# Kernel optimization log

Hardware: AMD Instinct MI355X
Metric: run time of the kernel (lower is better)

## Reference

```python
import jax, jax.numpy as jnp
import numpy as np

NUM_ITEMS = 1_000_000
DIM = 64
NUM_HEADS = 2
TEMPERATURE = 0.1
BATCH = 4096
MAX_LEN = 200
PAD_FRAC = 0.3  # fraction of positions set to padding (-1)


def setup_inputs() -> dict:
    key = jax.random.key(0)
    k_tab, k_q, k_hist, k_pad = jax.random.split(key, 4)
    item_table = jax.random.normal(k_tab, (NUM_ITEMS, DIM), dtype=jnp.float32)
    queries = 0.1 * jax.random.normal(k_q, (NUM_HEADS, DIM), dtype=jnp.float32)
    hist = jax.random.randint(k_hist, (BATCH, MAX_LEN), 0, NUM_ITEMS, dtype=jnp.int32)
    pad = jax.random.uniform(k_pad, (BATCH, MAX_LEN)) < PAD_FRAC
    history_indices = jnp.where(pad, jnp.int32(-1), hist)
    return {"history_indices": history_indices, "item_table": item_table, "queries": queries}


def reference(history_indices, item_table, queries) -> jnp.ndarray:
    num_items = item_table.shape[0]
    num_heads = queries.shape[0]
    hi = jnp.clip(history_indices, -1, num_items - 1)
    lookup = jnp.where(hi == -1, 0, hi)
    hist_embs = item_table[lookup]                              # [B, L, D] gather
    scores = jnp.einsum('bld,kd->bkl', hist_embs, queries)      # [B, K, L]
    valid = (hi != -1)[:, None, :]                              # [B, 1, L]
    scores = jnp.where(valid, scores, jnp.float32(-1e9))
    attn = jax.nn.softmax(scores / TEMPERATURE, axis=-1)        # [B, K, L]
    head_vecs = jnp.einsum('bkl,bld->bkd', attn, hist_embs)     # [B, K, D]
    user_vec = head_vecs.mean(axis=1) * num_heads               # == sum over heads
    return user_vec
```

## Files before the change

kernel.cpp:

```cpp
#include <hip/hip_runtime.h>

#define NUM_ITEMS   1000000
#define DIM         64
#define BATCH       4096
#define MAX_LEN     200
#define INV_TEMP    10.0f
#define NEG_BIG     -1e9f

__global__ __launch_bounds__(512, 8)
void attn_pool_kernel(const int* __restrict__ hist,
                      const float* __restrict__ table,
                      const float* __restrict__ queries,
                      float* __restrict__ out)
{
    __shared__ int   hidx[MAX_LEN];
    __shared__ float mrg[8][16][11];

    const int b    = blockIdx.x;
    const int t    = threadIdx.x;
    const int lane = t & 63;
    const int wave = t >> 6;
    const int g    = t >> 4;
    const int c4   = t & 15;

    if (t < MAX_LEN) {
        int idx = hist[b * MAX_LEN + t];
        if (idx >= NUM_ITEMS) idx = NUM_ITEMS - 1;
        hidx[t] = idx;
    }
    __syncthreads();

    const float4 q0 = *reinterpret_cast<const float4*>(&queries[c4 * 4]);
    const float4 q1 = *reinterpret_cast<const float4*>(&queries[DIM + c4 * 4]);

    float  n0 = 0.f, n1 = 0.f;
    float4 a0 = {0.f, 0.f, 0.f, 0.f}, a1 = {0.f, 0.f, 0.f, 0.f};

    #pragma unroll
    for (int it = 0; it < (MAX_LEN + 31) / 32; ++it) {
        const int l = it * 32 + g;
        if (l < MAX_LEN) {
            const int idx = hidx[l];
            const int row = idx < 0 ? 0 : idx;
            const float4 v = *reinterpret_cast<const float4*>(
                &table[(size_t)row * DIM + c4 * 4]);
            float s0 = v.x * q0.x + v.y * q0.y + v.z * q0.z + v.w * q0.w;
            float s1 = v.x * q1.x + v.y * q1.y + v.z * q1.z + v.w * q1.w;
            #pragma unroll
            for (int off = 1; off < 16; off <<= 1) {
                s0 += __shfl_xor(s0, off);
                s1 += __shfl_xor(s1, off);
            }
            if (idx < 0) { s0 = NEG_BIG; s1 = NEG_BIG; }
            const float p0 = __expf(s0 * INV_TEMP);
            const float p1 = __expf(s1 * INV_TEMP);
            n0 += p0;
            a0.x += p0 * v.x;  a0.y += p0 * v.y;
            a0.z += p0 * v.z;  a0.w += p0 * v.w;
            n1 += p1;
            a1.x += p1 * v.x;  a1.y += p1 * v.y;
            a1.z += p1 * v.z;  a1.w += p1 * v.w;
        }
    }

    #pragma unroll
    for (int off = 16; off <= 32; off <<= 1) {
        n0   += __shfl_xor(n0,   off);
        a0.x += __shfl_xor(a0.x, off);  a0.y += __shfl_xor(a0.y, off);
        a0.z += __shfl_xor(a0.z, off);  a0.w += __shfl_xor(a0.w, off);
        n1   += __shfl_xor(n1,   off);
        a1.x += __shfl_xor(a1.x, off);  a1.y += __shfl_xor(a1.y, off);
        a1.z += __shfl_xor(a1.z, off);  a1.w += __shfl_xor(a1.w, off);
    }

    if (lane < 16) {
        float* s = mrg[wave][c4];
        s[0] = n0;
        s[1] = a0.x; s[2] = a0.y; s[3] = a0.z; s[4] = a0.w;
        s[5] = n1;
        s[6] = a1.x; s[7] = a1.y; s[8] = a1.z; s[9] = a1.w;
    }
    __syncthreads();

    if (t < 16) {
        float  N0 = 0.f, N1 = 0.f;
        float4 A0 = {0.f, 0.f, 0.f, 0.f}, A1 = {0.f, 0.f, 0.f, 0.f};
        #pragma unroll
        for (int w = 0; w < 8; ++w) {
            const float* s = mrg[w][t];
            N0   += s[0];
            A0.x += s[1];  A0.y += s[2];  A0.z += s[3];  A0.w += s[4];
            N1   += s[5];
            A1.x += s[6];  A1.y += s[7];  A1.z += s[8];  A1.w += s[9];
        }
        const float i0 = 1.f / N0, i1 = 1.f / N1;
        float4 o;
        o.x = A0.x * i0 + A1.x * i1;
        o.y = A0.y * i0 + A1.y * i1;
        o.z = A0.z * i0 + A1.z * i1;
        o.w = A0.w * i0 + A1.w * i1;
        *reinterpret_cast<float4*>(&out[b * DIM + t * 4]) = o;
    }
}

extern "C" void kernel_launch(void* const* d_in, const int* in_sizes, int n_in,
                              void* d_out, int out_size, void* d_ws, size_t ws_size,
                              hipStream_t stream) {
    const int*   hist    = (const int*)d_in[0];
    const float* table   = (const float*)d_in[1];
    const float* queries = (const float*)d_in[2];
    float*       out     = (float*)d_out;

    attn_pool_kernel<<<BATCH, 512, 0, stream>>>(hist, table, queries, out);
}
```

Baseline: 38.41 us.

## Map one wavefront per batch row and drop cross-wave shared-memory reduction

Each 64-lane wave now processes a whole batch row (4 rows per 256-thread block), iterating over all 200 history positions four at a time. This removes the cross-wave shared-memory merge and its second barrier. Padded positions now get a zero weight directly instead of exp(-1e9). The cost is less parallelism per row: each wave runs a 50-iteration serial loop, so the kernel relies on occupancy and unrolling to keep enough gathers in flight.

```diff
diff --git a/kernel.cpp b/kernel.cpp
--- a/kernel.cpp
+++ b/kernel.cpp
@@ -5,28 +5,33 @@
 #define BATCH       4096
 #define MAX_LEN     200
 #define INV_TEMP    10.0f
-#define NEG_BIG     -1e9f
 
-__global__ __launch_bounds__(512, 8)
+__global__ __launch_bounds__(256, 4)
 void attn_pool_kernel(const int* __restrict__ hist,
                       const float* __restrict__ table,
                       const float* __restrict__ queries,
                       float* __restrict__ out)
 {
-    __shared__ int   hidx[MAX_LEN];
-    __shared__ float mrg[8][16][11];
+    __shared__ int sidx[4][MAX_LEN];
 
-    const int b    = blockIdx.x;
     const int t    = threadIdx.x;
     const int lane = t & 63;
     const int wave = t >> 6;
-    const int g    = t >> 4;
-    const int c4   = t & 15;
+    const int b    = blockIdx.x * 4 + wave;
+    const int g    = lane >> 4;
+    const int c4   = lane & 15;
 
-    if (t < MAX_LEN) {
-        int idx = hist[b * MAX_LEN + t];
+    const int* hb = hist + (size_t)b * MAX_LEN;
+    #pragma unroll
+    for (int k = 0; k < 3; ++k) {
+        int idx = hb[lane + 64 * k];
         if (idx >= NUM_ITEMS) idx = NUM_ITEMS - 1;
-        hidx[t] = idx;
+        sidx[wave][lane + 64 * k] = idx;
+    }
+    if (lane < MAX_LEN - 192) {
+        int idx = hb[192 + lane];
+        if (idx >= NUM_ITEMS) idx = NUM_ITEMS - 1;
+        sidx[wave][192 + lane] = idx;
     }
     __syncthreads();
 
@@ -36,31 +41,27 @@
     float  n0 = 0.f, n1 = 0.f;
     float4 a0 = {0.f, 0.f, 0.f, 0.f}, a1 = {0.f, 0.f, 0.f, 0.f};
 
-    #pragma unroll
-    for (int it = 0; it < (MAX_LEN + 31) / 32; ++it) {
-        const int l = it * 32 + g;
-        if (l < MAX_LEN) {
-            const int idx = hidx[l];
-            const int row = idx < 0 ? 0 : idx;
-            const float4 v = *reinterpret_cast<const float4*>(
-                &table[(size_t)row * DIM + c4 * 4]);
-            float s0 = v.x * q0.x + v.y * q0.y + v.z * q0.z + v.w * q0.w;
-            float s1 = v.x * q1.x + v.y * q1.y + v.z * q1.z + v.w * q1.w;
-            #pragma unroll
-            for (int off = 1; off < 16; off <<= 1) {
-                s0 += __shfl_xor(s0, off);
-                s1 += __shfl_xor(s1, off);
-            }
-            if (idx < 0) { s0 = NEG_BIG; s1 = NEG_BIG; }
-            const float p0 = __expf(s0 * INV_TEMP);
-            const float p1 = __expf(s1 * INV_TEMP);
-            n0 += p0;
-            a0.x += p0 * v.x;  a0.y += p0 * v.y;
-            a0.z += p0 * v.z;  a0.w += p0 * v.w;
-            n1 += p1;
-            a1.x += p1 * v.x;  a1.y += p1 * v.y;
-            a1.z += p1 * v.z;  a1.w += p1 * v.w;
+    #pragma unroll 10
+    for (int it = 0; it < MAX_LEN / 4; ++it) {
+        const int idx = sidx[wave][it * 4 + g];
+        const int row = idx < 0 ? 0 : idx;
+        const float4 v = *reinterpret_cast<const float4*>(
+            &table[(size_t)row * DIM + c4 * 4]);
+        float s0 = v.x * q0.x + v.y * q0.y + v.z * q0.z + v.w * q0.w;
+        float s1 = v.x * q1.x + v.y * q1.y + v.z * q1.z + v.w * q1.w;
+        #pragma unroll
+        for (int off = 1; off < 16; off <<= 1) {
+            s0 += __shfl_xor(s0, off);
+            s1 += __shfl_xor(s1, off);
         }
+        const float p0 = (idx < 0) ? 0.f : __expf(s0 * INV_TEMP);
+        const float p1 = (idx < 0) ? 0.f : __expf(s1 * INV_TEMP);
+        n0 += p0;
+        a0.x += p0 * v.x;  a0.y += p0 * v.y;
+        a0.z += p0 * v.z;  a0.w += p0 * v.w;
+        n1 += p1;
+        a1.x += p1 * v.x;  a1.y += p1 * v.y;
+        a1.z += p1 * v.z;  a1.w += p1 * v.w;
     }
 
     #pragma unroll
@@ -74,32 +75,13 @@
     }
 
     if (lane < 16) {
-        float* s = mrg[wave][c4];
-        s[0] = n0;
-        s[1] = a0.x; s[2] = a0.y; s[3] = a0.z; s[4] = a0.w;
-        s[5] = n1;
-        s[6] = a1.x; s[7] = a1.y; s[8] = a1.z; s[9] = a1.w;
-    }
-    __syncthreads();
-
-    if (t < 16) {
-        float  N0 = 0.f, N1 = 0.f;
-        float4 A0 = {0.f, 0.f, 0.f, 0.f}, A1 = {0.f, 0.f, 0.f, 0.f};
-        #pragma unroll
-        for (int w = 0; w < 8; ++w) {
-            const float* s = mrg[w][t];
-            N0   += s[0];
-            A0.x += s[1];  A0.y += s[2];  A0.z += s[3];  A0.w += s[4];
-            N1   += s[5];
-            A1.x += s[6];  A1.y += s[7];  A1.z += s[8];  A1.w += s[9];
-        }
-        const float i0 = 1.f / N0, i1 = 1.f / N1;
+        const float i0 = 1.f / n0, i1 = 1.f / n1;
         float4 o;
-        o.x = A0.x * i0 + A1.x * i1;
-        o.y = A0.y * i0 + A1.y * i1;
-        o.z = A0.z * i0 + A1.z * i1;
-        o.w = A0.w * i0 + A1.w * i1;
-        *reinterpret_cast<float4*>(&out[b * DIM + t * 4]) = o;
+        o.x = a0.x * i0 + a1.x * i1;
+        o.y = a0.y * i0 + a1.y * i1;
+        o.z = a0.z * i0 + a1.z * i1;
+        o.w = a0.w * i0 + a1.w * i1;
+        *reinterpret_cast<float4*>(&out[(size_t)b * DIM + lane * 4]) = o;
     }
 }
 
@@ -111,5 +93,5 @@
     const float* queries = (const float*)d_in[2];
     float*       out     = (float*)d_out;
 
-    attn_pool_kernel<<<BATCH, 512, 0, stream>>>(hist, table, queries, out);
+    attn_pool_kernel<<<BATCH / 4, 256, 0, stream>>>(hist, table, queries, out);
 }
```

Measured after the change: 33.24 us. -13.5%, faster.
